# Kernel tuning notes

Hardware: AMD Instinct MI355X
Metric: run time of the kernel (lower is better)

## Reference

```python
import jax, jax.numpy as jnp
import numpy as np

N_NODES = 100000
N_EDGES = 1600000
HIDDEN = 48
LAYERS = 4
ALPHA = 0.1
THETA = 0.5


def setup_inputs() -> dict:
    key = jax.random.key(0)
    ks = jax.random.split(key, 6)
    x = jax.random.normal(ks[0], (N_NODES, 3), dtype=jnp.float32)
    edge_index = jax.random.randint(ks[1], (2, N_EDGES), 0, N_NODES, dtype=jnp.int32)
    W0 = jax.random.normal(ks[2], (3, HIDDEN), dtype=jnp.float32) * 0.3
    b0 = jnp.zeros((HIDDEN,), dtype=jnp.float32)
    convW = jax.random.normal(ks[3], (LAYERS, HIDDEN, HIDDEN), dtype=jnp.float32) * (1.0 / np.sqrt(HIDDEN))
    W1 = jax.random.normal(ks[4], (HIDDEN, HIDDEN), dtype=jnp.float32) * (1.0 / np.sqrt(HIDDEN))
    b1 = jnp.zeros((HIDDEN,), dtype=jnp.float32)
    return {"x": x, "edge_index": edge_index, "W0": W0, "b0": b0,
            "convW": convW, "W1": W1, "b1": b1}


def reference(x, edge_index, W0, b0, convW, W1, b1):
    # lin0 + relu; x0 is the initial residual (dropout=0 / eval mode -> identity)
    h = jax.nn.relu(x @ W0 + b0)
    x0 = h
    src, dst = edge_index[0], edge_index[1]
    n = h.shape[0]
    for l in range(LAYERS):
        # sparse propagation: A @ h via gather + segment_sum (unit edge weights, normalize=False)
        agg = jax.ops.segment_sum(h[src], dst, num_segments=n)
        beta = float(np.log(THETA / (l + 1) + 1.0))
        # GCNII shared-weights branch: t = (1-alpha)*Ah + alpha*x0; out = (1-beta)*t + beta*(t @ W)
        t = (1.0 - ALPHA) * agg + ALPHA * x0
        h = jax.nn.relu((1.0 - beta) * t + beta * (t @ convW[l]))
    out = h @ W1 + b1
    return jax.nn.log_softmax(out, axis=-1)
```

## Files before the change

kernel.cpp:

```cpp
#include <hip/hip_runtime.h>
#include <math.h>

#define N_NODES 100000
#define N_EDGES 1600000
#define HID 48
#define ALPHA 0.1f

typedef unsigned short u16;
typedef unsigned int u32;

__device__ __forceinline__ float bf_lo(u32 u) { return __uint_as_float(u << 16); }
__device__ __forceinline__ float bf_hi(u32 u) { return __uint_as_float(u & 0xffff0000u); }
__device__ __forceinline__ float bf2f(u16 u) {
    return __uint_as_float(((u32)u) << 16);
}
__device__ __forceinline__ u16 f2bf(float f) {
    u32 b = __float_as_uint(f);
    b += 0x7fff + ((b >> 16) & 1);
    return (u16)(b >> 16);
}

__global__ __launch_bounds__(256) void lin0_k(const float* __restrict__ x, const float* __restrict__ W0,
                                              const float* __restrict__ b0, float* __restrict__ x0f,
                                              u16* __restrict__ h0) {
    int t = blockIdx.x * 256 + threadIdx.x;
    if (t >= N_NODES * HID) return;
    int node = t / HID, f = t % HID;
    float v = b0[f]
            + x[node * 3 + 0] * W0[0 * HID + f]
            + x[node * 3 + 1] * W0[1 * HID + f]
            + x[node * 3 + 2] * W0[2 * HID + f];
    v = v > 0.f ? v : 0.f;
    x0f[t] = v;
    h0[t] = f2bf(v);
}

__global__ __launch_bounds__(256) void count_k(const int* __restrict__ dst, int* __restrict__ deg,
                                               int* __restrict__ rank) {
    int e = blockIdx.x * 256 + threadIdx.x;
    if (e < N_EDGES) rank[e] = atomicAdd(&deg[dst[e]], 1);
}

__global__ __launch_bounds__(256) void scan1_k(const int* __restrict__ deg, int* __restrict__ rowptr,
                                               int* __restrict__ partial) {
    __shared__ int sums[256];
    int tid = threadIdx.x;
    int base = blockIdx.x * 2048 + tid * 8;
    int v[8]; int s = 0;
#pragma unroll
    for (int j = 0; j < 8; j++) { int idx = base + j; v[j] = (idx < N_NODES) ? deg[idx] : 0; s += v[j]; }
    sums[tid] = s; __syncthreads();
    for (int off = 1; off < 256; off <<= 1) {
        int t = (tid >= off) ? sums[tid - off] : 0;
        __syncthreads();
        sums[tid] += t;
        __syncthreads();
    }
    if (tid == 255) partial[blockIdx.x] = sums[255];
    int run = (tid > 0) ? sums[tid - 1] : 0;
#pragma unroll
    for (int j = 0; j < 8; j++) { int idx = base + j; if (idx < N_NODES) rowptr[idx] = run; run += v[j]; }
}

__global__ void scan2_k(int* __restrict__ partial, int* __restrict__ rowptr, int nblk) {
    int lane = threadIdx.x & 63;
    int v = (lane < nblk) ? partial[lane] : 0;
    for (int off = 1; off < 64; off <<= 1) {
        int t = __shfl_up(v, off);
        if (lane >= off) v += t;
    }
    int excl = __shfl_up(v, 1);
    if (lane == 0) excl = 0;
    if (lane < nblk) partial[lane] = excl;
    if (lane == 63) rowptr[N_NODES] = v;
}

__global__ __launch_bounds__(256) void scan3_k(int* __restrict__ rowptr, const int* __restrict__ partial) {
    int tid = threadIdx.x;
    int base = blockIdx.x * 2048 + tid * 8;
    int add = partial[blockIdx.x];
#pragma unroll
    for (int j = 0; j < 8; j++) {
        int idx = base + j;
        if (idx < N_NODES) rowptr[idx] += add;
    }
}

__global__ __launch_bounds__(256) void bucket_k(const int* __restrict__ src, const int* __restrict__ dst,
                                                const int* __restrict__ rank, const int* __restrict__ rowptr,
                                                int* __restrict__ ssrc) {
    int e = blockIdx.x * 256 + threadIdx.x;
    if (e < N_EDGES) {
        int d = dst[e];
        ssrc[rowptr[d] + rank[e]] = src[e];
    }
}

__global__ __launch_bounds__(256) void layer_k(const u16* __restrict__ h_in, const float* __restrict__ x0,
                                               const int* __restrict__ rowptr, const int* __restrict__ ssrc,
                                               const float* __restrict__ W, float beta,
                                               u16* __restrict__ h_out) {
    __shared__ float sW[2304];
    __shared__ float tbuf[4][48];
    int tid = threadIdx.x, wave = tid >> 6, lane = tid & 63;
#pragma unroll
    for (int i = 0; i < 9; i++) sW[i * 256 + tid] = W[i * 256 + tid];
    int node = blockIdx.x * 4 + wave;
    int chunk = lane & 7;
    int slot  = lane >> 3;
    bool act = chunk < 6;
    int cc = act ? chunk : 0;
    float a0 = 0.f, a1 = 0.f, a2 = 0.f, a3 = 0.f, a4 = 0.f, a5 = 0.f, a6 = 0.f, a7 = 0.f;
    if (node < N_NODES) {
        int e0 = rowptr[node], e1 = rowptr[node + 1];
        int e = e0;
        for (; e + 16 <= e1; e += 16) {
            int sA = ssrc[e + slot];
            int sB = ssrc[e + 8 + slot];
            const uint4 wA = *(const uint4*)(h_in + (size_t)sA * 48 + cc * 8);
            const uint4 wB = *(const uint4*)(h_in + (size_t)sB * 48 + cc * 8);
            a0 += bf_lo(wA.x) + bf_lo(wB.x);
            a1 += bf_hi(wA.x) + bf_hi(wB.x);
            a2 += bf_lo(wA.y) + bf_lo(wB.y);
            a3 += bf_hi(wA.y) + bf_hi(wB.y);
            a4 += bf_lo(wA.z) + bf_lo(wB.z);
            a5 += bf_hi(wA.z) + bf_hi(wB.z);
            a6 += bf_lo(wA.w) + bf_lo(wB.w);
            a7 += bf_hi(wA.w) + bf_hi(wB.w);
        }
        for (; e < e1; e += 8) {
            int idx = e + slot;
            int s = ssrc[idx < e1 ? idx : e];
            const uint4 w = *(const uint4*)(h_in + (size_t)s * 48 + cc * 8);
            if (idx < e1) {
                a0 += bf_lo(w.x); a1 += bf_hi(w.x);
                a2 += bf_lo(w.y); a3 += bf_hi(w.y);
                a4 += bf_lo(w.z); a5 += bf_hi(w.z);
                a6 += bf_lo(w.w); a7 += bf_hi(w.w);
            }
        }
#pragma unroll
        for (int off = 8; off <= 32; off <<= 1) {
            a0 += __shfl_xor(a0, off); a1 += __shfl_xor(a1, off);
            a2 += __shfl_xor(a2, off); a3 += __shfl_xor(a3, off);
            a4 += __shfl_xor(a4, off); a5 += __shfl_xor(a5, off);
            a6 += __shfl_xor(a6, off); a7 += __shfl_xor(a7, off);
        }
        if (act && slot == 0) {
            const float4 xv0 = *(const float4*)(x0 + (size_t)node * 48 + chunk * 8);
            const float4 xv1 = *(const float4*)(x0 + (size_t)node * 48 + chunk * 8 + 4);
            float4 t0, t1;
            t0.x = (1.f - ALPHA) * a0 + ALPHA * xv0.x;
            t0.y = (1.f - ALPHA) * a1 + ALPHA * xv0.y;
            t0.z = (1.f - ALPHA) * a2 + ALPHA * xv0.z;
            t0.w = (1.f - ALPHA) * a3 + ALPHA * xv0.w;
            t1.x = (1.f - ALPHA) * a4 + ALPHA * xv1.x;
            t1.y = (1.f - ALPHA) * a5 + ALPHA * xv1.y;
            t1.z = (1.f - ALPHA) * a6 + ALPHA * xv1.z;
            t1.w = (1.f - ALPHA) * a7 + ALPHA * xv1.w;
            ((float4*)tbuf[wave])[chunk * 2 + 0] = t0;
            ((float4*)tbuf[wave])[chunk * 2 + 1] = t1;
        }
    }
    __syncthreads();
    if (node < N_NODES && lane < 48) {
        const float4* t4 = (const float4*)tbuf[wave];
        float s = 0.f;
#pragma unroll
        for (int k4 = 0; k4 < 12; k4++) {
            float4 tv = t4[k4];
            s += tv.x * sW[(4 * k4 + 0) * 48 + lane] + tv.y * sW[(4 * k4 + 1) * 48 + lane]
               + tv.z * sW[(4 * k4 + 2) * 48 + lane] + tv.w * sW[(4 * k4 + 3) * 48 + lane];
        }
        float t = tbuf[wave][lane];
        float o = (1.f - beta) * t + beta * s;
        h_out[node * 48 + lane] = f2bf(o > 0.f ? o : 0.f);
    }
}

__global__ __launch_bounds__(256) void final_k(const u16* __restrict__ h, const float* __restrict__ W1,
                                               const float* __restrict__ b1, float* __restrict__ out) {
    __shared__ float sW[2304];
    __shared__ float sb[48];
    __shared__ float tbuf[4][48];
    int tid = threadIdx.x, wave = tid >> 6, lane = tid & 63;
#pragma unroll
    for (int i = 0; i < 9; i++) sW[i * 256 + tid] = W1[i * 256 + tid];
    if (tid < 48) sb[tid] = b1[tid];
    int node = blockIdx.x * 4 + wave;
    int f = lane < 48 ? lane : 0;
    if (node < N_NODES && lane < 48) tbuf[wave][lane] = bf2f(h[node * 48 + lane]);
    __syncthreads();
    float v = -INFINITY;
    if (node < N_NODES) {
        const float4* t4 = (const float4*)tbuf[wave];
        float s = sb[f];
#pragma unroll
        for (int k4 = 0; k4 < 12; k4++) {
            float4 tv = t4[k4];
            s += tv.x * sW[(4 * k4 + 0) * 48 + f] + tv.y * sW[(4 * k4 + 1) * 48 + f]
               + tv.z * sW[(4 * k4 + 2) * 48 + f] + tv.w * sW[(4 * k4 + 3) * 48 + f];
        }
        if (lane < 48) v = s;
    }
    float m = v;
    for (int off = 32; off >= 1; off >>= 1) m = fmaxf(m, __shfl_xor(m, off));
    float ex = (node < N_NODES && lane < 48) ? expf(v - m) : 0.f;
    float sum = ex;
    for (int off = 32; off >= 1; off >>= 1) sum += __shfl_xor(sum, off);
    if (node < N_NODES && lane < 48) {
        out[node * 48 + lane] = v - m - logf(sum);
    }
}

extern "C" void kernel_launch(void* const* d_in, const int* in_sizes, int n_in,
                              void* d_out, int out_size, void* d_ws, size_t ws_size,
                              hipStream_t stream) {
    const float* x     = (const float*)d_in[0];
    const int*   ei    = (const int*)d_in[1];
    const float* W0    = (const float*)d_in[2];
    const float* b0    = (const float*)d_in[3];
    const float* convW = (const float*)d_in[4];
    const float* W1    = (const float*)d_in[5];
    const float* b1    = (const float*)d_in[6];
    float* out = (float*)d_out;
    const int* src = ei;
    const int* dst = ei + N_EDGES;

    char* ws = (char*)d_ws;
    size_t off = 0;
    float* x0 = (float*)(ws + off); off += (size_t)N_NODES * 48 * 4;
    u16* hA   = (u16*)(ws + off);   off += (size_t)N_NODES * 48 * 2;
    u16* hB   = (u16*)(ws + off);   off += (size_t)N_NODES * 48 * 2;
    int* rank = (int*)hB;
    int* ssrc = (int*)(ws + off);   off += (size_t)N_EDGES * 4;
    int* rowptr = (int*)(ws + off); off += (size_t)(N_NODES + 1) * 4;
    off = (off + 255) & ~(size_t)255;
    int* cursorUnused = (int*)(ws + off); off += (size_t)N_NODES * 4;
    off = (off + 255) & ~(size_t)255;
    int* deg = (int*)(ws + off);    off += (size_t)N_NODES * 4;
    off = (off + 255) & ~(size_t)255;
    int* partial = (int*)(ws + off); off += 64 * 4;
    (void)cursorUnused;

    hipMemsetAsync(deg, 0, (size_t)N_NODES * 4, stream);

    lin0_k<<<18750, 256, 0, stream>>>(x, W0, b0, x0, hA);
    count_k<<<6250, 256, 0, stream>>>(dst, deg, rank);
    scan1_k<<<49, 256, 0, stream>>>(deg, rowptr, partial);
    scan2_k<<<1, 64, 0, stream>>>(partial, rowptr, 49);
    scan3_k<<<49, 256, 0, stream>>>(rowptr, partial);
    bucket_k<<<6250, 256, 0, stream>>>(src, dst, rank, rowptr, ssrc);

    const float betas[4] = { logf(1.5f), logf(1.25f), logf(7.f / 6.f), logf(1.125f) };

    layer_k<<<25000, 256, 0, stream>>>(hA, x0, rowptr, ssrc, convW + 0 * 2304, betas[0], hB);
    layer_k<<<25000, 256, 0, stream>>>(hB, x0, rowptr, ssrc, convW + 1 * 2304, betas[1], hA);
    layer_k<<<25000, 256, 0, stream>>>(hA, x0, rowptr, ssrc, convW + 2 * 2304, betas[2], hB);
    layer_k<<<25000, 256, 0, stream>>>(hB, x0, rowptr, ssrc, convW + 3 * 2304, betas[3], hA);
    final_k<<<25000, 256, 0, stream>>>(hA, W1, b1, out);
}
```

Measured before the change: 518.7 us.

## Pad node rows to 64 bf16, store x0 in bf16, transpose weights, deepen gather

Node feature rows are padded to a 128-byte stride so that each gathered row aligns to a cache line. The residual x0 is now held as bf16 in the same buffer as the first hidden state, which removes the separate fp32 copy. Weights are staged transposed in shared memory with a padded stride so each lane reads float4s. The edge gather loop now issues four loads per iteration instead of two, giving more memory parallelism. The padding adds bytes per row, and bf16 x0 adds small precision loss.

After: 545.1 us. +5.1%, slower.

```diff
diff --git a/kernel.cpp b/kernel.cpp
--- a/kernel.cpp
+++ b/kernel.cpp
@@ -4,7 +4,9 @@
 #define N_NODES 100000
 #define N_EDGES 1600000
 #define HID 48
+#define HPAD 64
 #define ALPHA 0.1f
+#define SW 52
 
 typedef unsigned short u16;
 typedef unsigned int u32;
@@ -19,20 +21,27 @@
     b += 0x7fff + ((b >> 16) & 1);
     return (u16)(b >> 16);
 }
+__device__ __forceinline__ u32 pack2(float a, float b) {
+    return (u32)f2bf(a) | ((u32)f2bf(b) << 16);
+}
 
 __global__ __launch_bounds__(256) void lin0_k(const float* __restrict__ x, const float* __restrict__ W0,
-                                              const float* __restrict__ b0, float* __restrict__ x0f,
-                                              u16* __restrict__ h0) {
+                                              const float* __restrict__ b0, u16* __restrict__ h0) {
     int t = blockIdx.x * 256 + threadIdx.x;
-    if (t >= N_NODES * HID) return;
-    int node = t / HID, f = t % HID;
-    float v = b0[f]
-            + x[node * 3 + 0] * W0[0 * HID + f]
-            + x[node * 3 + 1] * W0[1 * HID + f]
-            + x[node * 3 + 2] * W0[2 * HID + f];
-    v = v > 0.f ? v : 0.f;
-    x0f[t] = v;
-    h0[t] = f2bf(v);
+    if (t >= N_NODES * 6) return;
+    int node = t / 6, oct = t % 6;
+    float xv0 = x[node * 3 + 0], xv1 = x[node * 3 + 1], xv2 = x[node * 3 + 2];
+    float v[8];
+#pragma unroll
+    for (int j = 0; j < 8; j++) {
+        int f = oct * 8 + j;
+        float s = b0[f] + xv0 * W0[0 * HID + f] + xv1 * W0[1 * HID + f] + xv2 * W0[2 * HID + f];
+        v[j] = s > 0.f ? s : 0.f;
+    }
+    uint4 p;
+    p.x = pack2(v[0], v[1]); p.y = pack2(v[2], v[3]);
+    p.z = pack2(v[4], v[5]); p.w = pack2(v[6], v[7]);
+    *(uint4*)(h0 + (size_t)node * HPAD + oct * 8) = p;
 }
 
 __global__ __launch_bounds__(256) void count_k(const int* __restrict__ dst, int* __restrict__ deg,
@@ -96,15 +105,18 @@
     }
 }
 
-__global__ __launch_bounds__(256) void layer_k(const u16* __restrict__ h_in, const float* __restrict__ x0,
+__global__ __launch_bounds__(256) void layer_k(const u16* __restrict__ h_in, const u16* __restrict__ x0,
                                                const int* __restrict__ rowptr, const int* __restrict__ ssrc,
                                                const float* __restrict__ W, float beta,
                                                u16* __restrict__ h_out) {
-    __shared__ float sW[2304];
+    __shared__ float sWT[48 * SW];
     __shared__ float tbuf[4][48];
     int tid = threadIdx.x, wave = tid >> 6, lane = tid & 63;
 #pragma unroll
-    for (int i = 0; i < 9; i++) sW[i * 256 + tid] = W[i * 256 + tid];
+    for (int i = tid; i < 2304; i += 256) {
+        int r = i / 48, c = i % 48;
+        sWT[c * SW + r] = W[i];
+    }
     int node = blockIdx.x * 4 + wave;
     int chunk = lane & 7;
     int slot  = lane >> 3;
@@ -113,30 +125,31 @@
     float a0 = 0.f, a1 = 0.f, a2 = 0.f, a3 = 0.f, a4 = 0.f, a5 = 0.f, a6 = 0.f, a7 = 0.f;
     if (node < N_NODES) {
         int e0 = rowptr[node], e1 = rowptr[node + 1];
-        int e = e0;
-        for (; e + 16 <= e1; e += 16) {
-            int sA = ssrc[e + slot];
-            int sB = ssrc[e + 8 + slot];
-            const uint4 wA = *(const uint4*)(h_in + (size_t)sA * 48 + cc * 8);
-            const uint4 wB = *(const uint4*)(h_in + (size_t)sB * 48 + cc * 8);
-            a0 += bf_lo(wA.x) + bf_lo(wB.x);
-            a1 += bf_hi(wA.x) + bf_hi(wB.x);
-            a2 += bf_lo(wA.y) + bf_lo(wB.y);
-            a3 += bf_hi(wA.y) + bf_hi(wB.y);
-            a4 += bf_lo(wA.z) + bf_lo(wB.z);
-            a5 += bf_hi(wA.z) + bf_hi(wB.z);
-            a6 += bf_lo(wA.w) + bf_lo(wB.w);
-            a7 += bf_hi(wA.w) + bf_hi(wB.w);
-        }
-        for (; e < e1; e += 8) {
-            int idx = e + slot;
-            int s = ssrc[idx < e1 ? idx : e];
-            const uint4 w = *(const uint4*)(h_in + (size_t)s * 48 + cc * 8);
-            if (idx < e1) {
-                a0 += bf_lo(w.x); a1 += bf_hi(w.x);
-                a2 += bf_lo(w.y); a3 += bf_hi(w.y);
-                a4 += bf_lo(w.z); a5 += bf_hi(w.z);
-                a6 += bf_lo(w.w); a7 += bf_hi(w.w);
+        for (int e = e0; e < e1; e += 32) {
+            int i0 = e + slot, i1 = e + 8 + slot, i2 = e + 16 + slot, i3 = e + 24 + slot;
+            int s0 = ssrc[i0 < e1 ? i0 : e];
+            int s1 = ssrc[i1 < e1 ? i1 : e];
+            int s2 = ssrc[i2 < e1 ? i2 : e];
+            int s3 = ssrc[i3 < e1 ? i3 : e];
+            const uint4 w0 = *(const uint4*)(h_in + ((size_t)s0 << 6) + cc * 8);
+            const uint4 w1 = *(const uint4*)(h_in + ((size_t)s1 << 6) + cc * 8);
+            const uint4 w2 = *(const uint4*)(h_in + ((size_t)s2 << 6) + cc * 8);
+            const uint4 w3 = *(const uint4*)(h_in + ((size_t)s3 << 6) + cc * 8);
+            if (i0 < e1) {
+                a0 += bf_lo(w0.x); a1 += bf_hi(w0.x); a2 += bf_lo(w0.y); a3 += bf_hi(w0.y);
+                a4 += bf_lo(w0.z); a5 += bf_hi(w0.z); a6 += bf_lo(w0.w); a7 += bf_hi(w0.w);
+            }
+            if (i1 < e1) {
+                a0 += bf_lo(w1.x); a1 += bf_hi(w1.x); a2 += bf_lo(w1.y); a3 += bf_hi(w1.y);
+                a4 += bf_lo(w1.z); a5 += bf_hi(w1.z); a6 += bf_lo(w1.w); a7 += bf_hi(w1.w);
+            }
+            if (i2 < e1) {
+                a0 += bf_lo(w2.x); a1 += bf_hi(w2.x); a2 += bf_lo(w2.y); a3 += bf_hi(w2.y);
+                a4 += bf_lo(w2.z); a5 += bf_hi(w2.z); a6 += bf_lo(w2.w); a7 += bf_hi(w2.w);
+            }
+            if (i3 < e1) {
+                a0 += bf_lo(w3.x); a1 += bf_hi(w3.x); a2 += bf_lo(w3.y); a3 += bf_hi(w3.y);
+                a4 += bf_lo(w3.z); a5 += bf_hi(w3.z); a6 += bf_lo(w3.w); a7 += bf_hi(w3.w);
             }
         }
 #pragma unroll
@@ -147,17 +160,16 @@
             a6 += __shfl_xor(a6, off); a7 += __shfl_xor(a7, off);
         }
         if (act && slot == 0) {
-            const float4 xv0 = *(const float4*)(x0 + (size_t)node * 48 + chunk * 8);
-            const float4 xv1 = *(const float4*)(x0 + (size_t)node * 48 + chunk * 8 + 4);
+            const uint4 xv = *(const uint4*)(x0 + ((size_t)node << 6) + chunk * 8);
             float4 t0, t1;
-            t0.x = (1.f - ALPHA) * a0 + ALPHA * xv0.x;
-            t0.y = (1.f - ALPHA) * a1 + ALPHA * xv0.y;
-            t0.z = (1.f - ALPHA) * a2 + ALPHA * xv0.z;
-            t0.w = (1.f - ALPHA) * a3 + ALPHA * xv0.w;
-            t1.x = (1.f - ALPHA) * a4 + ALPHA * xv1.x;
-            t1.y = (1.f - ALPHA) * a5 + ALPHA * xv1.y;
-            t1.z = (1.f - ALPHA) * a6 + ALPHA * xv1.z;
-            t1.w = (1.f - ALPHA) * a7 + ALPHA * xv1.w;
+            t0.x = (1.f - ALPHA) * a0 + ALPHA * bf_lo(xv.x);
+            t0.y = (1.f - ALPHA) * a1 + ALPHA * bf_hi(xv.x);
+            t0.z = (1.f - ALPHA) * a2 + ALPHA * bf_lo(xv.y);
+            t0.w = (1.f - ALPHA) * a3 + ALPHA * bf_hi(xv.y);
+            t1.x = (1.f - ALPHA) * a4 + ALPHA * bf_lo(xv.z);
+            t1.y = (1.f - ALPHA) * a5 + ALPHA * bf_hi(xv.z);
+            t1.z = (1.f - ALPHA) * a6 + ALPHA * bf_lo(xv.w);
+            t1.w = (1.f - ALPHA) * a7 + ALPHA * bf_hi(xv.w);
             ((float4*)tbuf[wave])[chunk * 2 + 0] = t0;
             ((float4*)tbuf[wave])[chunk * 2 + 1] = t1;
         }
@@ -165,41 +177,46 @@
     __syncthreads();
     if (node < N_NODES && lane < 48) {
         const float4* t4 = (const float4*)tbuf[wave];
+        const float4* w4 = (const float4*)(sWT + lane * SW);
         float s = 0.f;
 #pragma unroll
         for (int k4 = 0; k4 < 12; k4++) {
             float4 tv = t4[k4];
-            s += tv.x * sW[(4 * k4 + 0) * 48 + lane] + tv.y * sW[(4 * k4 + 1) * 48 + lane]
-               + tv.z * sW[(4 * k4 + 2) * 48 + lane] + tv.w * sW[(4 * k4 + 3) * 48 + lane];
+            float4 wv = w4[k4];
+            s += tv.x * wv.x + tv.y * wv.y + tv.z * wv.z + tv.w * wv.w;
         }
         float t = tbuf[wave][lane];
         float o = (1.f - beta) * t + beta * s;
-        h_out[node * 48 + lane] = f2bf(o > 0.f ? o : 0.f);
+        h_out[(size_t)node * HPAD + lane] = f2bf(o > 0.f ? o : 0.f);
     }
 }
 
 __global__ __launch_bounds__(256) void final_k(const u16* __restrict__ h, const float* __restrict__ W1,
                                                const float* __restrict__ b1, float* __restrict__ out) {
-    __shared__ float sW[2304];
+    __shared__ float sWT[48 * SW];
     __shared__ float sb[48];
     __shared__ float tbuf[4][48];
     int tid = threadIdx.x, wave = tid >> 6, lane = tid & 63;
 #pragma unroll
-    for (int i = 0; i < 9; i++) sW[i * 256 + tid] = W1[i * 256 + tid];
+    for (int i = tid; i < 2304; i += 256) {
+        int r = i / 48, c = i % 48;
+        sWT[c * SW + r] = W1[i];
+    }
     if (tid < 48) sb[tid] = b1[tid];
     int node = blockIdx.x * 4 + wave;
     int f = lane < 48 ? lane : 0;
-    if (node < N_NODES && lane < 48) tbuf[wave][lane] = bf2f(h[node * 48 + lane]);
+    if (node < N_NODES && lane < 48) tbuf[wave][lane] = bf2f(h[(size_t)node * HPAD + lane]);
     __syncthreads();
     float v = -INFINITY;
     if (node < N_NODES) {
         const float4* t4 = (const float4*)tbuf[wave];
+        const float4* w4 = (const float4*)(sWT + f * SW);
         float s = sb[f];
 #pragma unroll
         for (int k4 = 0; k4 < 12; k4++) {
             float4 tv = t4[k4];
-            s += tv.x * sW[(4 * k4 + 0) * 48 + f] + tv.y * sW[(4 * k4 + 1) * 48 + f]
-               + tv.z * sW[(4 * k4 + 2) * 48 + f] + tv.w * sW[(4 * k4 + 3) * 48 + f];
+            float4 wv = w4[k4];
+            s += tv.x * wv.x + tv.y * wv.y + tv.z * wv.z + tv.w * wv.w;
         }
         if (lane < 48) v = s;
     }
@@ -229,23 +246,20 @@
 
     char* ws = (char*)d_ws;
     size_t off = 0;
-    float* x0 = (float*)(ws + off); off += (size_t)N_NODES * 48 * 4;
-    u16* hA   = (u16*)(ws + off);   off += (size_t)N_NODES * 48 * 2;
-    u16* hB   = (u16*)(ws + off);   off += (size_t)N_NODES * 48 * 2;
-    int* rank = (int*)hB;
+    u16* h0 = (u16*)(ws + off); off += (size_t)N_NODES * HPAD * 2;
+    u16* hA = (u16*)(ws + off); off += (size_t)N_NODES * HPAD * 2;
+    u16* hB = (u16*)(ws + off); off += (size_t)N_NODES * HPAD * 2;
+    int* rank = (int*)hA;
     int* ssrc = (int*)(ws + off);   off += (size_t)N_EDGES * 4;
     int* rowptr = (int*)(ws + off); off += (size_t)(N_NODES + 1) * 4;
-    off = (off + 255) & ~(size_t)255;
-    int* cursorUnused = (int*)(ws + off); off += (size_t)N_NODES * 4;
     off = (off + 255) & ~(size_t)255;
     int* deg = (int*)(ws + off);    off += (size_t)N_NODES * 4;
     off = (off + 255) & ~(size_t)255;
     int* partial = (int*)(ws + off); off += 64 * 4;
-    (void)cursorUnused;
 
     hipMemsetAsync(deg, 0, (size_t)N_NODES * 4, stream);
 
-    lin0_k<<<18750, 256, 0, stream>>>(x, W0, b0, x0, hA);
+    lin0_k<<<(N_NODES * 6 + 255) / 256, 256, 0, stream>>>(x, W0, b0, h0);
     count_k<<<6250, 256, 0, stream>>>(dst, deg, rank);
     scan1_k<<<49, 256, 0, stream>>>(deg, rowptr, partial);
     scan2_k<<<1, 64, 0, stream>>>(partial, rowptr, 49);
@@ -254,9 +268,9 @@
 
     const float betas[4] = { logf(1.5f), logf(1.25f), logf(7.f / 6.f), logf(1.125f) };
 
-    layer_k<<<25000, 256, 0, stream>>>(hA, x0, rowptr, ssrc, convW + 0 * 2304, betas[0], hB);
-    layer_k<<<25000, 256, 0, stream>>>(hB, x0, rowptr, ssrc, convW + 1 * 2304, betas[1], hA);
-    layer_k<<<25000, 256, 0, stream>>>(hA, x0, rowptr, ssrc, convW + 2 * 2304, betas[2], hB);
-    layer_k<<<25000, 256, 0, stream>>>(hB, x0, rowptr, ssrc, convW + 3 * 2304, betas[3], hA);
+    layer_k<<<25000, 256, 0, stream>>>(h0, h0, rowptr, ssrc, convW + 0 * 2304, betas[0], hB);
+    layer_k<<<25000, 256, 0, stream>>>(hB, h0, rowptr, ssrc, convW + 1 * 2304, betas[1], hA);
+    layer_k<<<25000, 256, 0, stream>>>(hA, h0, rowptr, ssrc, convW + 2 * 2304, betas[2], hB);
+    layer_k<<<25000, 256, 0, stream>>>(hB, h0, rowptr, ssrc, convW + 3 * 2304, betas[3], hA);
     final_k<<<25000, 256, 0, stream>>>(hA, W1, b1, out);
 }
```
